# Performance work log

Measured on AMD Instinct MI355X. Metric: run time of the kernel, lower is better.

The kernel has to match this reference:

```python
import jax, jax.numpy as jnp
import numpy as np

N, T, F, H = 20000, 64, 32, 64
E = 640000
G1, G2 = 64, 32


def _lstm_layer(x_seq, Wih, Whh, bih, bhh):
    # x_seq: [N, T, Fin] -> hs [N, T, H], PyTorch gate order i,f,g,o
    n, _, _ = x_seq.shape
    h_dim = Whh.shape[1]
    h0 = jnp.zeros((n, h_dim), x_seq.dtype)
    c0 = jnp.zeros((n, h_dim), x_seq.dtype)

    def step(carry, xt):
        h, c = carry
        gates = xt @ Wih.T + h @ Whh.T + bih + bhh
        i, f, g, o = jnp.split(gates, 4, axis=-1)
        c = jax.nn.sigmoid(f) * c + jax.nn.sigmoid(i) * jnp.tanh(g)
        h = jax.nn.sigmoid(o) * jnp.tanh(c)
        return (h, c), h

    (_, _), hs = jax.lax.scan(step, (h0, c0), jnp.swapaxes(x_seq, 0, 1))
    return jnp.swapaxes(hs, 0, 1)


def _gcn(h, src, dst, W, b):
    # GCNConv (PyG default): add self-loops, symmetric deg^-1/2 normalization
    n = h.shape[0]
    loop = jnp.arange(n)
    s = jnp.concatenate([src, loop])
    d = jnp.concatenate([dst, loop])
    deg = jax.ops.segment_sum(jnp.ones_like(d, dtype=h.dtype), d, num_segments=n)
    dinv = jnp.where(deg > 0, deg ** -0.5, 0.0)
    norm = dinv[s] * dinv[d]
    xw = h @ W                      # [n, out]
    msg = xw[s] * norm[:, None]     # gather on source nodes
    return jax.ops.segment_sum(msg, d, num_segments=n) + b


def setup_inputs() -> dict:
    key = jax.random.key(0)
    ks = jax.random.split(key, 16)
    s = 0.1
    inp = {
        "x": jax.random.normal(ks[0], (N, T, F), jnp.float32),
        "stock_ids": jax.random.randint(ks[1], (N,), 0, N),
        "edge_index": jax.random.randint(ks[2], (2, E), 0, N),
        # LSTM layer 0
        "Wih0": jax.random.normal(ks[3], (4 * H, F), jnp.float32) * s,
        "Whh0": jax.random.normal(ks[4], (4 * H, H), jnp.float32) * s,
        "bih0": jnp.zeros((4 * H,), jnp.float32),
        "bhh0": jnp.zeros((4 * H,), jnp.float32),
        # LSTM layer 1
        "Wih1": jax.random.normal(ks[5], (4 * H, H), jnp.float32) * s,
        "Whh1": jax.random.normal(ks[6], (4 * H, H), jnp.float32) * s,
        "bih1": jnp.zeros((4 * H,), jnp.float32),
        "bhh1": jnp.zeros((4 * H,), jnp.float32),
        # GCN layers
        "gcn1_W": jax.random.normal(ks[7], (H, G1), jnp.float32) * s,
        "gcn1_b": jnp.zeros((G1,), jnp.float32),
        "gcn2_W": jax.random.normal(ks[8], (G1, G2), jnp.float32) * s,
        "gcn2_b": jnp.zeros((G2,), jnp.float32),
        # head
        "fc_W": jax.random.normal(ks[9], (1, G2), jnp.float32) * s,
        "fc_b": jnp.zeros((1,), jnp.float32),
    }
    return inp


def reference(x, stock_ids, edge_index, Wih0, Whh0, bih0, bhh0,
              Wih1, Whh1, bih1, bhh1, gcn1_W, gcn1_b, gcn2_W, gcn2_b,
              fc_W, fc_b):
    # 2-layer LSTM (eval mode: inter-layer dropout is identity)
    h1 = _lstm_layer(x, Wih0, Whh0, bih0, bhh0)
    h2 = _lstm_layer(h1, Wih1, Whh1, bih1, bhh1)
    h = h2[:, -1, :]                              # [N, H]
    src, dst = edge_index[0], edge_index[1]
    g = jax.nn.relu(_gcn(h, src, dst, gcn1_W, gcn1_b))
    g = jax.nn.relu(_gcn(g, src, dst, gcn2_W, gcn2_b))
    node_features = g[stock_ids]                  # [B, 32]
    out = node_features @ fc_W.T + fc_b           # [B, 1]
    return out.squeeze(-1)
```

## Files before the change

kernel.cpp:

```cpp
#include <hip/hip_runtime.h>
#include <math.h>

#define TT 64
#define FF 32
#define HH 64
#define NN 16
#define GG1 64
#define GG2 32

typedef float f32x4 __attribute__((ext_vector_type(4)));
typedef short bf16x8 __attribute__((ext_vector_type(8)));

__device__ __forceinline__ float fexp2(float x){ return __builtin_amdgcn_exp2f(x); }
__device__ __forceinline__ float frcp (float x){ return __builtin_amdgcn_rcpf(x); }
#define L2E 1.442695041f
__device__ __forceinline__ float sigm_nb(float v, float nb){
  return frcp(1.0f + fexp2(fmaf(v, -L2E, nb)));
}
__device__ __forceinline__ float tanh_b(float v, float b2){
  return fmaf(-2.0f, frcp(1.0f + fexp2(fmaf(v, 2.0f*L2E, b2))), 1.0f);
}
__device__ __forceinline__ float tanh0(float v){
  return fmaf(-2.0f, frcp(1.0f + fexp2(2.0f*L2E*v)), 1.0f);
}

__device__ __forceinline__ float xor8(float v){
  int a = __builtin_bit_cast(int, v);
  int b = __builtin_amdgcn_update_dpp(0, a, 0x128, 0xF, 0xF, true);
  return __builtin_bit_cast(float, b);
}

__device__ __forceinline__ unsigned short bf16rn(float x){
  unsigned u = __builtin_bit_cast(unsigned, x);
  return (unsigned short)((u + 0x7FFFu + ((u >> 16) & 1u)) >> 16);
}
__device__ __forceinline__ void split2(float x, unsigned short& h, unsigned short& l){
  unsigned u = __builtin_bit_cast(unsigned, x);
  unsigned hr = (u + 0x7FFFu + ((u >> 16) & 1u)) & 0xFFFF0000u;
  h = (unsigned short)(hr >> 16);
  l = bf16rn(x - __builtin_bit_cast(float, hr));
}
__device__ __forceinline__ void split_pk(float a, float b, unsigned& hi2, unsigned& lo2){
  asm("v_cvt_pk_bf16_f32 %0, %1, %2" : "=v"(hi2) : "v"(a), "v"(b));
  float ha = __builtin_bit_cast(float, hi2 << 16);
  float hb = __builtin_bit_cast(float, hi2 & 0xFFFF0000u);
  float la = a - ha, lb = b - hb;
  asm("v_cvt_pk_bf16_f32 %0, %1, %2" : "=v"(lo2) : "v"(la), "v"(lb));
}

#define PIN(v) asm volatile("" : "+v"(v))
#define MFMA(acc, a, b) (acc) = __builtin_amdgcn_mfma_f32_16x16x32_bf16((a), (b), (acc), 0, 0, 0)

__device__ __forceinline__ void wsplit(const float* p, bf16x8& hi, bf16x8& lo){
  float4 a = *(const float4*)p;
  float4 b = *(const float4*)(p + 4);
  unsigned short h, s;
  split2(a.x,h,s); hi[0]=(short)h; lo[0]=(short)s;
  split2(a.y,h,s); hi[1]=(short)h; lo[1]=(short)s;
  split2(a.z,h,s); hi[2]=(short)h; lo[2]=(short)s;
  split2(a.w,h,s); hi[3]=(short)h; lo[3]=(short)s;
  split2(b.x,h,s); hi[4]=(short)h; lo[4]=(short)s;
  split2(b.y,h,s); hi[5]=(short)h; lo[5]=(short)s;
  split2(b.z,h,s); hi[6]=(short)h; lo[6]=(short)s;
  split2(b.w,h,s); hi[7]=(short)h; lo[7]=(short)s;
}

__global__ __launch_bounds__(1024, 4)
void lstm_mfma(const float* __restrict__ x,
    const float* __restrict__ Wih0, const float* __restrict__ Whh0,
    const float* __restrict__ bih0, const float* __restrict__ bhh0,
    const float* __restrict__ Wih1, const float* __restrict__ Whh1,
    const float* __restrict__ bih1, const float* __restrict__ bhh1,
    float* __restrict__ hout, int n)
{
  const int tid  = threadIdx.x;
  const int wv   = tid >> 6;
  const int role = wv >> 3;
  const int w    = wv & 7;
  const int l    = tid & 63;
  const int lr   = l & 15;
  const int lg   = l >> 4;
  const int nA   = blockIdx.x * NN;
  int avail = n - nA; if (avail > NN) avail = NN;

  __shared__ short Ax[2][2][16][40];
  __shared__ short H0[2][2][16][88];
  __shared__ short H1[2][2][16][88];

  const int jm   = lr & 7;
  const bool lo8 = (lr < 8);
  const int col0 = lo8 ? (8*w + jm) : (64  + 8*w + jm);
  const int col1 = lo8 ? (128 + 8*w + jm) : (192 + 8*w + jm);

  bf16x8 Wh[2][4], Wl[2][4];
  if (role == 0){
#pragma unroll
    for (int h = 0; h < 2; ++h){
      const int col = h ? col1 : col0;
      wsplit(Wih0 + col*FF + 8*lg,      Wh[h][0], Wl[h][0]);
      wsplit(Whh0 + col*HH + 8*lg,      Wh[h][1], Wl[h][1]);
      wsplit(Whh0 + col*HH + 32 + 8*lg, Wh[h][2], Wl[h][2]);
      Wh[h][3] = Wh[h][2]; Wl[h][3] = Wl[h][2];
    }
  } else {
#pragma unroll
    for (int h = 0; h < 2; ++h){
      const int col = h ? col1 : col0;
      wsplit(Wih1 + col*HH + 8*lg,      Wh[h][0], Wl[h][0]);
      wsplit(Wih1 + col*HH + 32 + 8*lg, Wh[h][1], Wl[h][1]);
      wsplit(Whh1 + col*HH + 8*lg,      Wh[h][2], Wl[h][2]);
      wsplit(Whh1 + col*HH + 32 + 8*lg, Wh[h][3], Wl[h][3]);
    }
  }
#pragma unroll
  for (int h = 0; h < 2; ++h)
#pragma unroll
    for (int k = 0; k < 4; ++k){ PIN(Wh[h][k]); PIN(Wl[h][k]); }

  const int m = 8*w + jm;
  const float* bi = role ? bih1 : bih0;
  const float* bh = role ? bhh1 : bhh0;
  const float nb_i = -L2E      * (bi[m      ] + bh[m      ]);
  const float nb_f = -L2E      * (bi[m +  64] + bh[m +  64]);
  const float b2_g =  2.0f*L2E * (bi[m + 128] + bh[m + 128]);
  const float nb_o = -L2E      * (bi[m + 192] + bh[m + 192]);

  {
    short* p0 = &H0[0][0][0][0];
    short* p1 = &H1[0][0][0][0];
    for (int i = tid; i < 2*2*16*88; i += 1024){ p0[i] = 0; p1[i] = 0; }
    if (tid < 512){
      const int xnd = tid >> 5, xf = tid & 31;
      float v = (xnd < avail) ? x[((size_t)(nA+xnd)*TT + 0)*FF + xf] : 0.0f;
      unsigned short hh, hl; split2(v, hh, hl);
      Ax[0][0][xnd][xf] = (short)hh;
      Ax[0][1][xnd][xf] = (short)hl;
    }
  }
  const int na = 4*lg + (lo8 ? 0 : 2);
  const int nb = na + 1;
  float ca = 0.0f, cb = 0.0f;
  const f32x4 Z = {0.f, 0.f, 0.f, 0.f};
  __syncthreads();

  for (int t = 0; t < TT; ++t){
    const int rd0 = (t & 1) ^ 1;
    const int wr0 =  t & 1;
    const int rd1 =  t & 1;
    const int wr1 = (t & 1) ^ 1;

    if (role == 0){
      const int xnd = tid >> 5, xf = tid & 31;
      const int tp = t + 1;
      float xv = 0.0f;
      if (tp < TT && xnd < avail) xv = x[((size_t)(nA+xnd)*TT + tp)*FF + xf];

      bf16x8 axh  = *(const bf16x8*)&Ax[t&1][0][lr][8*lg];
      bf16x8 axl  = *(const bf16x8*)&Ax[t&1][1][lr][8*lg];
      bf16x8 h0ah = *(const bf16x8*)&H0[rd0][0][lr][8*lg];
      bf16x8 h0al = *(const bf16x8*)&H0[rd0][1][lr][8*lg];
      bf16x8 h0bh = *(const bf16x8*)&H0[rd0][0][lr][32+8*lg];
      bf16x8 h0bl = *(const bf16x8*)&H0[rd0][1][lr][32+8*lg];

      __builtin_amdgcn_s_setprio(1);
      f32x4 A0, A1;
      A0 = __builtin_amdgcn_mfma_f32_16x16x32_bf16(axl, Wh[0][0], Z, 0, 0, 0);
      A1 = __builtin_amdgcn_mfma_f32_16x16x32_bf16(axl, Wh[1][0], Z, 0, 0, 0);
      MFMA(A0, axh,  Wl[0][0]); MFMA(A0, axh,  Wh[0][0]);
      MFMA(A1, axh,  Wl[1][0]); MFMA(A1, axh,  Wh[1][0]);
      MFMA(A0, h0al, Wh[0][1]); MFMA(A0, h0ah, Wl[0][1]); MFMA(A0, h0ah, Wh[0][1]);
      MFMA(A1, h0al, Wh[1][1]); MFMA(A1, h0ah, Wl[1][1]); MFMA(A1, h0ah, Wh[1][1]);
      MFMA(A0, h0bl, Wh[0][2]); MFMA(A0, h0bh, Wl[0][2]); MFMA(A0, h0bh, Wh[0][2]);
      MFMA(A1, h0bl, Wh[1][2]); MFMA(A1, h0bh, Wl[1][2]); MFMA(A1, h0bh, Wh[1][2]);
      __builtin_amdgcn_s_setprio(0);

      if (tp < TT){
        unsigned short hh, hl; split2(xv, hh, hl);
        Ax[tp&1][0][xnd][xf] = (short)hh;
        Ax[tp&1][1][xnd][xf] = (short)hl;
      }

      f32x4 s0, s1;
      s0[0]=xor8(A0[0]); s0[1]=xor8(A0[1]); s0[2]=xor8(A0[2]); s0[3]=xor8(A0[3]);
      s1[0]=xor8(A1[0]); s1[1]=xor8(A1[1]); s1[2]=xor8(A1[2]); s1[3]=xor8(A1[3]);
      float gi_a = lo8 ? A0[0] : s0[2],  gi_b = lo8 ? A0[1] : s0[3];
      float gf_a = lo8 ? s0[0] : A0[2],  gf_b = lo8 ? s0[1] : A0[3];
      float gg_a = lo8 ? A1[0] : s1[2],  gg_b = lo8 ? A1[1] : s1[3];
      float go_a = lo8 ? s1[0] : A1[2],  go_b = lo8 ? s1[1] : A1[3];
      ca = sigm_nb(gf_a, nb_f)*ca + sigm_nb(gi_a, nb_i)*tanh_b(gg_a, b2_g);
      float ha = sigm_nb(go_a, nb_o)*tanh0(ca);
      cb = sigm_nb(gf_b, nb_f)*cb + sigm_nb(gi_b, nb_i)*tanh_b(gg_b, b2_g);
      float hb = sigm_nb(go_b, nb_o)*tanh0(cb);
      unsigned hi2, lo2; split_pk(ha, hb, hi2, lo2);
      H0[wr0][0][na][m] = (short)(hi2 & 0xFFFF);
      H0[wr0][0][nb][m] = (short)(hi2 >> 16);
      H0[wr0][1][na][m] = (short)(lo2 & 0xFFFF);
      H0[wr0][1][nb][m] = (short)(lo2 >> 16);
    }
    else if (t > 0){
      bf16x8 h0ah = *(const bf16x8*)&H0[rd0][0][lr][8*lg];
      bf16x8 h0al = *(const bf16x8*)&H0[rd0][1][lr][8*lg];
      bf16x8 h0bh = *(const bf16x8*)&H0[rd0][0][lr][32+8*lg];
      bf16x8 h0bl = *(const bf16x8*)&H0[rd0][1][lr][32+8*lg];

      __builtin_amdgcn_s_setprio(1);
      f32x4 D0, D1;
      D0 = __builtin_amdgcn_mfma_f32_16x16x32_bf16(h0al, Wh[0][0], Z, 0, 0, 0);
      D1 = __builtin_amdgcn_mfma_f32_16x16x32_bf16(h0al, Wh[1][0], Z, 0, 0, 0);
      MFMA(D0, h0ah, Wl[0][0]); MFMA(D0, h0ah, Wh[0][0]);
      MFMA(D1, h0ah, Wl[1][0]); MFMA(D1, h0ah, Wh[1][0]);
      MFMA(D0, h0bl, Wh[0][1]); MFMA(D0, h0bh, Wl[0][1]); MFMA(D0, h0bh, Wh[0][1]);
      MFMA(D1, h0bl, Wh[1][1]); MFMA(D1, h0bh, Wl[1][1]); MFMA(D1, h0bh, Wh[1][1]);
      bf16x8 h1ah = *(const bf16x8*)&H1[rd1][0][lr][8*lg];
      bf16x8 h1al = *(const bf16x8*)&H1[rd1][1][lr][8*lg];
      bf16x8 h1bh = *(const bf16x8*)&H1[rd1][0][lr][32+8*lg];
      bf16x8 h1bl = *(const bf16x8*)&H1[rd1][1][lr][32+8*lg];
      MFMA(D0, h1al, Wh[0][2]); MFMA(D0, h1ah, Wl[0][2]); MFMA(D0, h1ah, Wh[0][2]);
      MFMA(D1, h1al, Wh[1][2]); MFMA(D1, h1ah, Wl[1][2]); MFMA(D1, h1ah, Wh[1][2]);
      MFMA(D0, h1bl, Wh[0][3]); MFMA(D0, h1bh, Wl[0][3]); MFMA(D0, h1bh, Wh[0][3]);
      MFMA(D1, h1bl, Wh[1][3]); MFMA(D1, h1bh, Wl[1][3]); MFMA(D1, h1bh, Wh[1][3]);
      __builtin_amdgcn_s_setprio(0);

      f32x4 s0, s1;
      s0[0]=xor8(D0[0]); s0[1]=xor8(D0[1]); s0[2]=xor8(D0[2]); s0[3]=xor8(D0[3]);
      s1[0]=xor8(D1[0]); s1[1]=xor8(D1[1]); s1[2]=xor8(D1[2]); s1[3]=xor8(D1[3]);
      float gi_a = lo8 ? D0[0] : s0[2],  gi_b = lo8 ? D0[1] : s0[3];
      float gf_a = lo8 ? s0[0] : D0[2],  gf_b = lo8 ? s0[1] : D0[3];
      float gg_a = lo8 ? D1[0] : s1[2],  gg_b = lo8 ? D1[1] : s1[3];
      float go_a = lo8 ? s1[0] : D1[2],  go_b = lo8 ? s1[1] : D1[3];
      ca = sigm_nb(gf_a, nb_f)*ca + sigm_nb(gi_a, nb_i)*tanh_b(gg_a, b2_g);
      float ha = sigm_nb(go_a, nb_o)*tanh0(ca);
      cb = sigm_nb(gf_b, nb_f)*cb + sigm_nb(gi_b, nb_i)*tanh_b(gg_b, b2_g);
      float hb = sigm_nb(go_b, nb_o)*tanh0(cb);
      unsigned hi2, lo2; split_pk(ha, hb, hi2, lo2);
      H1[wr1][0][na][m] = (short)(hi2 & 0xFFFF);
      H1[wr1][0][nb][m] = (short)(hi2 >> 16);
      H1[wr1][1][na][m] = (short)(lo2 & 0xFFFF);
      H1[wr1][1][nb][m] = (short)(lo2 >> 16);
    }
    __syncthreads();
  }

  if (role == 1){
    const int rd0 = (TT-1) & 1;
    const int rd1 =  TT & 1;
    bf16x8 h0ah = *(const bf16x8*)&H0[rd0][0][lr][8*lg];
    bf16x8 h0al = *(const bf16x8*)&H0[rd0][1][lr][8*lg];
    bf16x8 h0bh = *(const bf16x8*)&H0[rd0][0][lr][32+8*lg];
    bf16x8 h0bl = *(const bf16x8*)&H0[rd0][1][lr][32+8*lg];
    bf16x8 h1ah = *(const bf16x8*)&H1[rd1][0][lr][8*lg];
    bf16x8 h1al = *(const bf16x8*)&H1[rd1][1][lr][8*lg];
    bf16x8 h1bh = *(const bf16x8*)&H1[rd1][0][lr][32+8*lg];
    bf16x8 h1bl = *(const bf16x8*)&H1[rd1][1][lr][32+8*lg];
    f32x4 D0 = __builtin_amdgcn_mfma_f32_16x16x32_bf16(h0al, Wh[0][0], Z, 0, 0, 0);
    f32x4 D1 = __builtin_amdgcn_mfma_f32_16x16x32_bf16(h0al, Wh[1][0], Z, 0, 0, 0);
    MFMA(D0, h0ah, Wl[0][0]); MFMA(D0, h0ah, Wh[0][0]);
    MFMA(D1, h0ah, Wl[1][0]); MFMA(D1, h0ah, Wh[1][0]);
    MFMA(D0, h0bl, Wh[0][1]); MFMA(D0, h0bh, Wl[0][1]); MFMA(D0, h0bh, Wh[0][1]);
    MFMA(D1, h0bl, Wh[1][1]); MFMA(D1, h0bh, Wl[1][1]); MFMA(D1, h0bh, Wh[1][1]);
    MFMA(D0, h1al, Wh[0][2]); MFMA(D0, h1ah, Wl[0][2]); MFMA(D0, h1ah, Wh[0][2]);
    MFMA(D1, h1al, Wh[1][2]); MFMA(D1, h1ah, Wl[1][2]); MFMA(D1, h1ah, Wh[1][2]);
    MFMA(D0, h1bl, Wh[0][3]); MFMA(D0, h1bh, Wl[0][3]); MFMA(D0, h1bh, Wh[0][3]);
    MFMA(D1, h1bl, Wh[1][3]); MFMA(D1, h1bh, Wl[1][3]); MFMA(D1, h1bh, Wh[1][3]);

    f32x4 s0, s1;
    s0[0]=xor8(D0[0]); s0[1]=xor8(D0[1]); s0[2]=xor8(D0[2]); s0[3]=xor8(D0[3]);
    s1[0]=xor8(D1[0]); s1[1]=xor8(D1[1]); s1[2]=xor8(D1[2]); s1[3]=xor8(D1[3]);
    float gi_a = lo8 ? D0[0] : s0[2],  gi_b = lo8 ? D0[1] : s0[3];
    float gf_a = lo8 ? s0[0] : D0[2],  gf_b = lo8 ? s0[1] : D0[3];
    float gg_a = lo8 ? D1[0] : s1[2],  gg_b = lo8 ? D1[1] : s1[3];
    float go_a = lo8 ? s1[0] : D1[2],  go_b = lo8 ? s1[1] : D1[3];
    ca = sigm_nb(gf_a, nb_f)*ca + sigm_nb(gi_a, nb_i)*tanh_b(gg_a, b2_g);
    float ha = sigm_nb(go_a, nb_o)*tanh0(ca);
    cb = sigm_nb(gf_b, nb_f)*cb + sigm_nb(gi_b, nb_i)*tanh_b(gg_b, b2_g);
    float hb = sigm_nb(go_b, nb_o)*tanh0(cb);
    if (nA + na < n) hout[(size_t)(nA+na)*HH + m] = ha;
    if (nA + nb < n) hout[(size_t)(nA+nb)*HH + m] = hb;
  }
}

__global__ void k_count(const int* __restrict__ dst, int E, int* __restrict__ cnt)
{
  int e = blockIdx.x * blockDim.x + threadIdx.x;
  if (e < E) atomicAdd(&cnt[dst[e]], 1);
}

__global__ void k_scan_build(const int* __restrict__ cnt, int n,
                             int* __restrict__ offs, int* __restrict__ cursor,
                             float* __restrict__ dinv)
{
  __shared__ int part[1024];
  const int tid = threadIdx.x;
  const int per = (n + 1023) >> 10;
  const int base = tid * per;
  int s = 0;
  for (int i = 0; i < per; ++i) { int idx = base + i; if (idx < n) s += cnt[idx]; }
  part[tid] = s;
  __syncthreads();
  for (int off = 1; off < 1024; off <<= 1) {
    int v = 0;
    if (tid >= off) v = part[tid - off];
    __syncthreads();
    part[tid] += v;
    __syncthreads();
  }
  int run = part[tid] - s;
  for (int i = 0; i < per; ++i) {
    int idx = base + i;
    if (idx < n) {
      offs[idx] = run; cursor[idx] = run;
      int c = cnt[idx];
      dinv[idx] = 1.0f / sqrtf((float)(c + 1));
      run += c;
    }
  }
}

__global__ void k_fill(const int* __restrict__ src, const int* __restrict__ dst,
                       int E, int* __restrict__ cursor, int* __restrict__ csr)
{
  int e = blockIdx.x * blockDim.x + threadIdx.x;
  if (e < E) {
    int d = dst[e];
    int pos = atomicAdd(&cursor[d], 1);
    csr[pos] = src[e];
  }
}

template <int K, int M>
__global__ void k_xw(const float* __restrict__ A, const float* __restrict__ W,
                     float* __restrict__ out, int n)
{
  int idx = blockIdx.x * blockDim.x + threadIdx.x;
  int row = idx / M, col = idx % M;
  if (row >= n) return;
  const float* a = A + (size_t)row * K;
  float acc = 0.0f;
#pragma unroll
  for (int k = 0; k < K; ++k) acc = fmaf(a[k], W[k*M + col], acc);
  out[(size_t)row*M + col] = acc;
}

__global__ void k_agg_x2(const float* __restrict__ xw, const int* __restrict__ offs,
                         const int* __restrict__ cnt, const int* __restrict__ csr,
                         const float* __restrict__ dinv, const float* __restrict__ b,
                         const float* __restrict__ W2,
                         float* __restrict__ g1out, float* __restrict__ xw2out, int n)
{
  __shared__ float sg[4][GG1];
  const int nd   = threadIdx.x >> 6;
  const int lane = threadIdx.x & 63;
  const int node = blockIdx.x * 4 + nd;
  if (node < n) {
    const float di = dinv[node];
    float acc = xw[(size_t)node*GG1 + lane] * di * di;
    const int s0 = offs[node], e0 = s0 + cnt[node];
    for (int p = s0; p < e0; ++p) {
      int s = csr[p];
      acc = fmaf(xw[(size_t)s*GG1 + lane], dinv[s] * di, acc);
    }
    float val = fmaxf(acc + b[lane], 0.0f);
    g1out[(size_t)node*GG1 + lane] = val;
    sg[nd][lane] = val;
  }
  __syncthreads();
  if (node < n && lane < GG2) {
    float a2 = 0.0f;
#pragma unroll
    for (int k = 0; k < GG1; ++k) a2 = fmaf(sg[nd][k], W2[k*GG2 + lane], a2);
    xw2out[(size_t)node*GG2 + lane] = a2;
  }
}

template <int FD>
__global__ void k_agg(const float* __restrict__ xw, const int* __restrict__ offs,
                      const int* __restrict__ cnt, const int* __restrict__ csr,
                      const float* __restrict__ dinv, const float* __restrict__ b,
                      float* __restrict__ out, int n)
{
  int gidx = blockIdx.x * blockDim.x + threadIdx.x;
  int node = gidx / FD, lane = gidx % FD;
  if (node >= n) return;
  const float di = dinv[node];
  float acc = xw[(size_t)node*FD + lane] * di * di;
  const int s0 = offs[node], e0 = s0 + cnt[node];
  for (int p = s0; p < e0; ++p) {
    int s = csr[p];
    acc = fmaf(xw[(size_t)s*FD + lane], dinv[s] * di, acc);
  }
  out[(size_t)node*FD + lane] = fmaxf(acc + b[lane], 0.0f);
}

__global__ void k_fc(const float* __restrict__ g2, const int* __restrict__ sid,
                     const float* __restrict__ fcW, const float* __restrict__ fcb,
                     float* __restrict__ out, int n)
{
  int i = blockIdx.x * blockDim.x + threadIdx.x;
  if (i >= n) return;
  const float* row = g2 + (size_t)sid[i] * GG2;
  float acc = fcb[0];
#pragma unroll
  for (int f = 0; f < GG2; ++f) acc = fmaf(row[f], fcW[f], acc);
  out[i] = acc;
}

extern "C" void kernel_launch(void* const* d_in, const int* in_sizes, int n_in,
                              void* d_out, int out_size, void* d_ws, size_t ws_size,
                              hipStream_t stream)
{
  const float* x    = (const float*)d_in[0];
  const int*   sid  = (const int*)  d_in[1];
  const int*   eidx = (const int*)  d_in[2];
  const float* Wih0 = (const float*)d_in[3];
  const float* Whh0 = (const float*)d_in[4];
  const float* bih0 = (const float*)d_in[5];
  const float* bhh0 = (const float*)d_in[6];
  const float* Wih1 = (const float*)d_in[7];
  const float* Whh1 = (const float*)d_in[8];
  const float* bih1 = (const float*)d_in[9];
  const float* bhh1 = (const float*)d_in[10];
  const float* g1W  = (const float*)d_in[11];
  const float* g1b  = (const float*)d_in[12];
  const float* g2W  = (const float*)d_in[13];
  const float* g2b  = (const float*)d_in[14];
  const float* fcW  = (const float*)d_in[15];
  const float* fcb  = (const float*)d_in[16];

  const int n = in_sizes[1];
  const int E = in_sizes[2] / 2;
  float* out = (float*)d_out;

  char* w = (char*)d_ws;
  auto carve = [&](size_t bytes) -> void* {
    void* p = (void*)w; w += (bytes + 255) & ~(size_t)255; return p;
  };
  float* hfin   = (float*)carve((size_t)n * HH * 4);
  int*   cnt    = (int*)  carve((size_t)n * 4);
  int*   offs   = (int*)  carve((size_t)n * 4);
  int*   cursor = (int*)  carve((size_t)n * 4);
  float* dinv   = (float*)carve((size_t)n * 4);
  int*   csr    = (int*)  carve((size_t)E * 4);
  float* xw1    = (float*)carve((size_t)n * GG1 * 4);
  float* g1     = (float*)carve((size_t)n * GG1 * 4);
  float* xw2    = (float*)carve((size_t)n * GG2 * 4);
  float* g2     = (float*)carve((size_t)n * GG2 * 4);

  const int* src = eidx;
  const int* dst = eidx + E;

  lstm_mfma<<<(n + NN - 1) / NN, 1024, 0, stream>>>(x, Wih0, Whh0, bih0, bhh0,
                                                    Wih1, Whh1, bih1, bhh1, hfin, n);

  hipMemsetAsync(cnt, 0, (size_t)n * 4, stream);
  k_count<<<(E + 255) / 256, 256, 0, stream>>>(dst, E, cnt);
  k_scan_build<<<1, 1024, 0, stream>>>(cnt, n, offs, cursor, dinv);
  k_fill<<<(E + 255) / 256, 256, 0, stream>>>(src, dst, E, cursor, csr);

  k_xw<HH, GG1><<<((size_t)n * GG1 + 255) / 256, 256, 0, stream>>>(hfin, g1W, xw1, n);
  k_agg_x2<<<(n + 3) / 4, 256, 0, stream>>>(xw1, offs, cnt, csr, dinv, g1b, g2W, g1, xw2, n);

  k_agg<GG2><<<((size_t)n * GG2 + 255) / 256, 256, 0, stream>>>(xw2, offs, cnt, csr, dinv, g2b, g2, n);

  k_fc<<<(n + 255) / 256, 256, 0, stream>>>(g2, sid, fcW, fcb, out, n);
}
```

Measured before the change: 683.4 us.

## Split LSTM timestep into two phases so layer-0 MFMA overlaps layer-1 activations

Each timestep is split into two barrier-separated phases. In the first phase, layer-0 waves issue their MFMAs while layer-1 waves apply the gate nonlinearities to the previous step's accumulators. In the second phase, layer-0 does its nonlinearity while layer-1 issues its MFMAs. This pairs matrix-core work from one role with transcendental ALU work from the other, and lets H1 drop its double buffer. The cost is an extra __syncthreads per timestep and an extra epilogue phase, which adds sync overhead on a latency-bound recurrence.

```diff
diff --git a/kernel.cpp b/kernel.cpp
--- a/kernel.cpp
+++ b/kernel.cpp
@@ -85,7 +85,7 @@
 
   __shared__ short Ax[2][2][16][40];
   __shared__ short H0[2][2][16][88];
-  __shared__ short H1[2][2][16][88];
+  __shared__ short H1[2][16][88];
 
   const int jm   = lr & 7;
   const bool lo8 = (lr < 8);
@@ -127,8 +127,9 @@
 
   {
     short* p0 = &H0[0][0][0][0];
-    short* p1 = &H1[0][0][0][0];
-    for (int i = tid; i < 2*2*16*88; i += 1024){ p0[i] = 0; p1[i] = 0; }
+    for (int i = tid; i < 2*2*16*88; i += 1024) p0[i] = 0;
+    short* p1 = &H1[0][0][0];
+    for (int i = tid; i < 2*16*88; i += 1024) p1[i] = 0;
     if (tid < 512){
       const int xnd = tid >> 5, xf = tid & 31;
       float v = (xnd < avail) ? x[((size_t)(nA+xnd)*TT + 0)*FF + xf] : 0.0f;
@@ -140,19 +141,19 @@
   const int na = 4*lg + (lo8 ? 0 : 2);
   const int nb = na + 1;
   float ca = 0.0f, cb = 0.0f;
+  f32x4 D0 = {0.f,0.f,0.f,0.f}, D1 = {0.f,0.f,0.f,0.f};
   const f32x4 Z = {0.f, 0.f, 0.f, 0.f};
   __syncthreads();
 
   for (int t = 0; t < TT; ++t){
     const int rd0 = (t & 1) ^ 1;
     const int wr0 =  t & 1;
-    const int rd1 =  t & 1;
-    const int wr1 = (t & 1) ^ 1;
+    f32x4 A0, A1;
+    float xv = 0.0f;
 
     if (role == 0){
       const int xnd = tid >> 5, xf = tid & 31;
       const int tp = t + 1;
-      float xv = 0.0f;
       if (tp < TT && xnd < avail) xv = x[((size_t)(nA+xnd)*TT + tp)*FF + xf];
 
       bf16x8 axh  = *(const bf16x8*)&Ax[t&1][0][lr][8*lg];
@@ -163,7 +164,6 @@
       bf16x8 h0bl = *(const bf16x8*)&H0[rd0][1][lr][32+8*lg];
 
       __builtin_amdgcn_s_setprio(1);
-      f32x4 A0, A1;
       A0 = __builtin_amdgcn_mfma_f32_16x16x32_bf16(axl, Wh[0][0], Z, 0, 0, 0);
       A1 = __builtin_amdgcn_mfma_f32_16x16x32_bf16(axl, Wh[1][0], Z, 0, 0, 0);
       MFMA(A0, axh,  Wl[0][0]); MFMA(A0, axh,  Wh[0][0]);
@@ -173,13 +173,28 @@
       MFMA(A0, h0bl, Wh[0][2]); MFMA(A0, h0bh, Wl[0][2]); MFMA(A0, h0bh, Wh[0][2]);
       MFMA(A1, h0bl, Wh[1][2]); MFMA(A1, h0bh, Wl[1][2]); MFMA(A1, h0bh, Wh[1][2]);
       __builtin_amdgcn_s_setprio(0);
-
-      if (tp < TT){
-        unsigned short hh, hl; split2(xv, hh, hl);
-        Ax[tp&1][0][xnd][xf] = (short)hh;
-        Ax[tp&1][1][xnd][xf] = (short)hl;
-      }
-
+    }
+    else if (t >= 2){
+      f32x4 s0, s1;
+      s0[0]=xor8(D0[0]); s0[1]=xor8(D0[1]); s0[2]=xor8(D0[2]); s0[3]=xor8(D0[3]);
+      s1[0]=xor8(D1[0]); s1[1]=xor8(D1[1]); s1[2]=xor8(D1[2]); s1[3]=xor8(D1[3]);
+      float gi_a = lo8 ? D0[0] : s0[2],  gi_b = lo8 ? D0[1] : s0[3];
+      float gf_a = lo8 ? s0[0] : D0[2],  gf_b = lo8 ? s0[1] : D0[3];
+      float gg_a = lo8 ? D1[0] : s1[2],  gg_b = lo8 ? D1[1] : s1[3];
+      float go_a = lo8 ? s1[0] : D1[2],  go_b = lo8 ? s1[1] : D1[3];
+      ca = sigm_nb(gf_a, nb_f)*ca + sigm_nb(gi_a, nb_i)*tanh_b(gg_a, b2_g);
+      float ha = sigm_nb(go_a, nb_o)*tanh0(ca);
+      cb = sigm_nb(gf_b, nb_f)*cb + sigm_nb(gi_b, nb_i)*tanh_b(gg_b, b2_g);
+      float hb = sigm_nb(go_b, nb_o)*tanh0(cb);
+      unsigned hi2, lo2; split_pk(ha, hb, hi2, lo2);
+      H1[0][na][m] = (short)(hi2 & 0xFFFF);
+      H1[0][nb][m] = (short)(hi2 >> 16);
+      H1[1][na][m] = (short)(lo2 & 0xFFFF);
+      H1[1][nb][m] = (short)(lo2 >> 16);
+    }
+    __syncthreads();
+
+    if (role == 0){
       f32x4 s0, s1;
       s0[0]=xor8(A0[0]); s0[1]=xor8(A0[1]); s0[2]=xor8(A0[2]); s0[3]=xor8(A0[3]);
       s1[0]=xor8(A1[0]); s1[1]=xor8(A1[1]); s1[2]=xor8(A1[2]); s1[3]=xor8(A1[3]);
@@ -196,73 +211,41 @@
       H0[wr0][0][nb][m] = (short)(hi2 >> 16);
       H0[wr0][1][na][m] = (short)(lo2 & 0xFFFF);
       H0[wr0][1][nb][m] = (short)(lo2 >> 16);
-    }
-    else if (t > 0){
+      const int xnd = tid >> 5, xf = tid & 31;
+      const int tp = t + 1;
+      if (tp < TT){
+        unsigned short hh, hl; split2(xv, hh, hl);
+        Ax[tp&1][0][xnd][xf] = (short)hh;
+        Ax[tp&1][1][xnd][xf] = (short)hl;
+      }
+    }
+    else if (t >= 1){
       bf16x8 h0ah = *(const bf16x8*)&H0[rd0][0][lr][8*lg];
       bf16x8 h0al = *(const bf16x8*)&H0[rd0][1][lr][8*lg];
       bf16x8 h0bh = *(const bf16x8*)&H0[rd0][0][lr][32+8*lg];
       bf16x8 h0bl = *(const bf16x8*)&H0[rd0][1][lr][32+8*lg];
 
       __builtin_amdgcn_s_setprio(1);
-      f32x4 D0, D1;
       D0 = __builtin_amdgcn_mfma_f32_16x16x32_bf16(h0al, Wh[0][0], Z, 0, 0, 0);
       D1 = __builtin_amdgcn_mfma_f32_16x16x32_bf16(h0al, Wh[1][0], Z, 0, 0, 0);
       MFMA(D0, h0ah, Wl[0][0]); MFMA(D0, h0ah, Wh[0][0]);
       MFMA(D1, h0ah, Wl[1][0]); MFMA(D1, h0ah, Wh[1][0]);
       MFMA(D0, h0bl, Wh[0][1]); MFMA(D0, h0bh, Wl[0][1]); MFMA(D0, h0bh, Wh[0][1]);
       MFMA(D1, h0bl, Wh[1][1]); MFMA(D1, h0bh, Wl[1][1]); MFMA(D1, h0bh, Wh[1][1]);
-      bf16x8 h1ah = *(const bf16x8*)&H1[rd1][0][lr][8*lg];
-      bf16x8 h1al = *(const bf16x8*)&H1[rd1][1][lr][8*lg];
-      bf16x8 h1bh = *(const bf16x8*)&H1[rd1][0][lr][32+8*lg];
-      bf16x8 h1bl = *(const bf16x8*)&H1[rd1][1][lr][32+8*lg];
+      bf16x8 h1ah = *(const bf16x8*)&H1[0][lr][8*lg];
+      bf16x8 h1al = *(const bf16x8*)&H1[1][lr][8*lg];
+      bf16x8 h1bh = *(const bf16x8*)&H1[0][lr][32+8*lg];
+      bf16x8 h1bl = *(const bf16x8*)&H1[1][lr][32+8*lg];
       MFMA(D0, h1al, Wh[0][2]); MFMA(D0, h1ah, Wl[0][2]); MFMA(D0, h1ah, Wh[0][2]);
       MFMA(D1, h1al, Wh[1][2]); MFMA(D1, h1ah, Wl[1][2]); MFMA(D1, h1ah, Wh[1][2]);
       MFMA(D0, h1bl, Wh[0][3]); MFMA(D0, h1bh, Wl[0][3]); MFMA(D0, h1bh, Wh[0][3]);
       MFMA(D1, h1bl, Wh[1][3]); MFMA(D1, h1bh, Wl[1][3]); MFMA(D1, h1bh, Wh[1][3]);
       __builtin_amdgcn_s_setprio(0);
-
-      f32x4 s0, s1;
-      s0[0]=xor8(D0[0]); s0[1]=xor8(D0[1]); s0[2]=xor8(D0[2]); s0[3]=xor8(D0[3]);
-      s1[0]=xor8(D1[0]); s1[1]=xor8(D1[1]); s1[2]=xor8(D1[2]); s1[3]=xor8(D1[3]);
-      float gi_a = lo8 ? D0[0] : s0[2],  gi_b = lo8 ? D0[1] : s0[3];
-      float gf_a = lo8 ? s0[0] : D0[2],  gf_b = lo8 ? s0[1] : D0[3];
-      float gg_a = lo8 ? D1[0] : s1[2],  gg_b = lo8 ? D1[1] : s1[3];
-      float go_a = lo8 ? s1[0] : D1[2],  go_b = lo8 ? s1[1] : D1[3];
-      ca = sigm_nb(gf_a, nb_f)*ca + sigm_nb(gi_a, nb_i)*tanh_b(gg_a, b2_g);
-      float ha = sigm_nb(go_a, nb_o)*tanh0(ca);
-      cb = sigm_nb(gf_b, nb_f)*cb + sigm_nb(gi_b, nb_i)*tanh_b(gg_b, b2_g);
-      float hb = sigm_nb(go_b, nb_o)*tanh0(cb);
-      unsigned hi2, lo2; split_pk(ha, hb, hi2, lo2);
-      H1[wr1][0][na][m] = (short)(hi2 & 0xFFFF);
-      H1[wr1][0][nb][m] = (short)(hi2 >> 16);
-      H1[wr1][1][na][m] = (short)(lo2 & 0xFFFF);
-      H1[wr1][1][nb][m] = (short)(lo2 >> 16);
     }
     __syncthreads();
   }
 
   if (role == 1){
-    const int rd0 = (TT-1) & 1;
-    const int rd1 =  TT & 1;
-    bf16x8 h0ah = *(const bf16x8*)&H0[rd0][0][lr][8*lg];
-    bf16x8 h0al = *(const bf16x8*)&H0[rd0][1][lr][8*lg];
-    bf16x8 h0bh = *(const bf16x8*)&H0[rd0][0][lr][32+8*lg];
-    bf16x8 h0bl = *(const bf16x8*)&H0[rd0][1][lr][32+8*lg];
-    bf16x8 h1ah = *(const bf16x8*)&H1[rd1][0][lr][8*lg];
-    bf16x8 h1al = *(const bf16x8*)&H1[rd1][1][lr][8*lg];
-    bf16x8 h1bh = *(const bf16x8*)&H1[rd1][0][lr][32+8*lg];
-    bf16x8 h1bl = *(const bf16x8*)&H1[rd1][1][lr][32+8*lg];
-    f32x4 D0 = __builtin_amdgcn_mfma_f32_16x16x32_bf16(h0al, Wh[0][0], Z, 0, 0, 0);
-    f32x4 D1 = __builtin_amdgcn_mfma_f32_16x16x32_bf16(h0al, Wh[1][0], Z, 0, 0, 0);
-    MFMA(D0, h0ah, Wl[0][0]); MFMA(D0, h0ah, Wh[0][0]);
-    MFMA(D1, h0ah, Wl[1][0]); MFMA(D1, h0ah, Wh[1][0]);
-    MFMA(D0, h0bl, Wh[0][1]); MFMA(D0, h0bh, Wl[0][1]); MFMA(D0, h0bh, Wh[0][1]);
-    MFMA(D1, h0bl, Wh[1][1]); MFMA(D1, h0bh, Wl[1][1]); MFMA(D1, h0bh, Wh[1][1]);
-    MFMA(D0, h1al, Wh[0][2]); MFMA(D0, h1ah, Wl[0][2]); MFMA(D0, h1ah, Wh[0][2]);
-    MFMA(D1, h1al, Wh[1][2]); MFMA(D1, h1ah, Wl[1][2]); MFMA(D1, h1ah, Wh[1][2]);
-    MFMA(D0, h1bl, Wh[0][3]); MFMA(D0, h1bh, Wl[0][3]); MFMA(D0, h1bh, Wh[0][3]);
-    MFMA(D1, h1bl, Wh[1][3]); MFMA(D1, h1bh, Wl[1][3]); MFMA(D1, h1bh, Wh[1][3]);
-
     f32x4 s0, s1;
     s0[0]=xor8(D0[0]); s0[1]=xor8(D0[1]); s0[2]=xor8(D0[2]); s0[3]=xor8(D0[3]);
     s1[0]=xor8(D1[0]); s1[1]=xor8(D1[1]); s1[2]=xor8(D1[2]); s1[3]=xor8(D1[3]);
@@ -270,6 +253,45 @@
     float gf_a = lo8 ? s0[0] : D0[2],  gf_b = lo8 ? s0[1] : D0[3];
     float gg_a = lo8 ? D1[0] : s1[2],  gg_b = lo8 ? D1[1] : s1[3];
     float go_a = lo8 ? s1[0] : D1[2],  go_b = lo8 ? s1[1] : D1[3];
+    ca = sigm_nb(gf_a, nb_f)*ca + sigm_nb(gi_a, nb_i)*tanh_b(gg_a, b2_g);
+    float ha = sigm_nb(go_a, nb_o)*tanh0(ca);
+    cb = sigm_nb(gf_b, nb_f)*cb + sigm_nb(gi_b, nb_i)*tanh_b(gg_b, b2_g);
+    float hb = sigm_nb(go_b, nb_o)*tanh0(cb);
+    unsigned hi2, lo2; split_pk(ha, hb, hi2, lo2);
+    H1[0][na][m] = (short)(hi2 & 0xFFFF);
+    H1[0][nb][m] = (short)(hi2 >> 16);
+    H1[1][na][m] = (short)(lo2 & 0xFFFF);
+    H1[1][nb][m] = (short)(lo2 >> 16);
+  }
+  __syncthreads();
+  if (role == 1){
+    const int rd0 = (TT-1) & 1;
+    bf16x8 h0ah = *(const bf16x8*)&H0[rd0][0][lr][8*lg];
+    bf16x8 h0al = *(const bf16x8*)&H0[rd0][1][lr][8*lg];
+    bf16x8 h0bh = *(const bf16x8*)&H0[rd0][0][lr][32+8*lg];
+    bf16x8 h0bl = *(const bf16x8*)&H0[rd0][1][lr][32+8*lg];
+    bf16x8 h1ah = *(const bf16x8*)&H1[0][lr][8*lg];
+    bf16x8 h1al = *(const bf16x8*)&H1[1][lr][8*lg];
+    bf16x8 h1bh = *(const bf16x8*)&H1[0][lr][32+8*lg];
+    bf16x8 h1bl = *(const bf16x8*)&H1[1][lr][32+8*lg];
+    f32x4 E0 = __builtin_amdgcn_mfma_f32_16x16x32_bf16(h0al, Wh[0][0], Z, 0, 0, 0);
+    f32x4 E1 = __builtin_amdgcn_mfma_f32_16x16x32_bf16(h0al, Wh[1][0], Z, 0, 0, 0);
+    MFMA(E0, h0ah, Wl[0][0]); MFMA(E0, h0ah, Wh[0][0]);
+    MFMA(E1, h0ah, Wl[1][0]); MFMA(E1, h0ah, Wh[1][0]);
+    MFMA(E0, h0bl, Wh[0][1]); MFMA(E0, h0bh, Wl[0][1]); MFMA(E0, h0bh, Wh[0][1]);
+    MFMA(E1, h0bl, Wh[1][1]); MFMA(E1, h0bh, Wl[1][1]); MFMA(E1, h0bh, Wh[1][1]);
+    MFMA(E0, h1al, Wh[0][2]); MFMA(E0, h1ah, Wl[0][2]); MFMA(E0, h1ah, Wh[0][2]);
+    MFMA(E1, h1al, Wh[1][2]); MFMA(E1, h1ah, Wl[1][2]); MFMA(E1, h1ah, Wh[1][2]);
+    MFMA(E0, h1bl, Wh[0][3]); MFMA(E0, h1bh, Wl[0][3]); MFMA(E0, h1bh, Wh[0][3]);
+    MFMA(E1, h1bl, Wh[1][3]); MFMA(E1, h1bh, Wl[1][3]); MFMA(E1, h1bh, Wh[1][3]);
+
+    f32x4 s0, s1;
+    s0[0]=xor8(E0[0]); s0[1]=xor8(E0[1]); s0[2]=xor8(E0[2]); s0[3]=xor8(E0[3]);
+    s1[0]=xor8(E1[0]); s1[1]=xor8(E1[1]); s1[2]=xor8(E1[2]); s1[3]=xor8(E1[3]);
+    float gi_a = lo8 ? E0[0] : s0[2],  gi_b = lo8 ? E0[1] : s0[3];
+    float gf_a = lo8 ? s0[0] : E0[2],  gf_b = lo8 ? s0[1] : E0[3];
+    float gg_a = lo8 ? E1[0] : s1[2],  gg_b = lo8 ? E1[1] : s1[3];
+    float go_a = lo8 ? s1[0] : E1[2],  go_b = lo8 ? s1[1] : E1[3];
     ca = sigm_nb(gf_a, nb_f)*ca + sigm_nb(gi_a, nb_i)*tanh_b(gg_a, b2_g);
     float ha = sigm_nb(go_a, nb_o)*tanh0(ca);
     cb = sigm_nb(gf_b, nb_f)*cb + sigm_nb(gi_b, nb_i)*tanh_b(gg_b, b2_g);
```

Result: no change. 684.5 us (+0.2%).
